# Kernel optimization log

Hardware: AMD Instinct MI355X
Metric: run time of the kernel (lower is better)

## Reference

```python
import jax, jax.numpy as jnp
import numpy as np

B, D, R, F = 4096, 14, 7, 768

def setup_inputs() -> dict:
    key = jax.random.key(0)
    ks = jax.random.split(key, 8)
    s = 1.0 / np.sqrt(F)
    return {
        "features": jax.random.normal(ks[0], (B, D, F), dtype=jnp.float32),
        "region_embeddings": jax.random.normal(ks[1], (R, F), dtype=jnp.float32),
        "Wq": jax.random.uniform(ks[2], (F, F), jnp.float32, -s, s),
        "bq": jnp.zeros((F,), jnp.float32),
        "Wk": jax.random.uniform(ks[3], (F, F), jnp.float32, -s, s),
        "bk": jnp.zeros((F,), jnp.float32),
        "Wv": jax.random.uniform(ks[4], (F, F), jnp.float32, -s, s),
        "bv": jnp.zeros((F,), jnp.float32),
        "region_weights": jnp.array([1.0, 1.0, 1.2, 1.5, 1.3, 1.1, 1.4], dtype=jnp.float32),
    }

def reference(features, region_embeddings, Wq, bq, Wk, bk, Wv, bv, region_weights):
    scale = features.shape[-1] ** -0.5
    # Q: [B, D, F]; K, V: [R, F] (shared across batch, broadcast instead of expand)
    Q = jnp.einsum('bdf,gf->bdg', features, Wq) + bq
    K = region_embeddings @ Wk.T + bk   # [R, F]
    V = region_embeddings @ Wv.T + bv   # [R, F]
    scores = jnp.einsum('bdf,rf->bdr', Q, K) * scale      # [B, D, R]
    scores = scores * region_weights[None, None, :]        # elementwise region bias
    attn = jax.nn.softmax(scores, axis=-1)                 # [B, D, R]
    attended = jnp.einsum('bdr,rf->bdf', attn, V)          # [B, D, F]
    return attended, attn
```

## Files before the change

kernel.cpp:

```cpp
#include <hip/hip_runtime.h>
#include <math.h>

#define FDIM 768
#define RNUM 7
#define BDIM 4096
#define DDIM 14
#define BD (BDIM * DDIM)
#define RF (RNUM * FDIM)
#define NCHUNK 4
#define GPC (FDIM / NCHUNK)
#define SCALE 0.03608439182435161f

#define CBLK 896
#define NW (CBLK * 8)
#define CITER 4

typedef float f4v __attribute__((ext_vector_type(4)));

#define DPP_ADD(x, ctrl)                                                      \
    x += __int_as_float(__builtin_amdgcn_update_dpp(                          \
        0, __float_as_int(x), ctrl, 0xf, 0xf, true))

__device__ __forceinline__ float wave_sum(float x)
{
    DPP_ADD(x, 0x111);
    DPP_ADD(x, 0x112);
    DPP_ADD(x, 0x114);
    DPP_ADD(x, 0x118);
    DPP_ADD(x, 0x142);
    DPP_ADD(x, 0x143);
    return __int_as_float(__builtin_amdgcn_readlane(__float_as_int(x), 63));
}

__global__ __launch_bounds__(512) void kv_kernel(
    const float* __restrict__ re,
    const float* __restrict__ Wk, const float* __restrict__ bk,
    const float* __restrict__ Wv, const float* __restrict__ bv,
    float* __restrict__ Kbuf, float* __restrict__ Vbuf,
    float* __restrict__ Kp, float* __restrict__ c_acc)
{
    __shared__ float re_s[RF];
    int tid = threadIdx.x;
    for (int i = tid; i < RF / 4; i += 512)
        ((float4*)re_s)[i] = ((const float4*)re)[i];

    if (blockIdx.x == 0) {
        float4 z = make_float4(0.f, 0.f, 0.f, 0.f);
        for (int i = tid; i < RF / 4; i += 512)
            ((float4*)Kp)[i] = z;
        if (tid < RNUM) c_acc[tid] = 0.f;
    }
    __syncthreads();

    int lane = tid & 63;
    int gwave = (int)((blockIdx.x * 512 + tid) >> 6);
    int which = gwave >= FDIM;
    int f = gwave - which * FDIM;

    const float4* W4 = (const float4*)((which ? Wv : Wk) + (size_t)f * FDIM);
    float4 w0 = W4[lane];
    float4 w1 = W4[lane + 64];
    float4 w2 = W4[lane + 128];

    float s[RNUM];
#pragma unroll
    for (int r = 0; r < RNUM; ++r) {
        const float4* a4 = (const float4*)(re_s + r * FDIM);
        float4 a0 = a4[lane];
        float4 a1 = a4[lane + 64];
        float4 a2 = a4[lane + 128];
        float p = a0.x * w0.x + a0.y * w0.y + a0.z * w0.z + a0.w * w0.w
                + a1.x * w1.x + a1.y * w1.y + a1.z * w1.z + a1.w * w1.w
                + a2.x * w2.x + a2.y * w2.y + a2.z * w2.z + a2.w * w2.w;
        s[r] = wave_sum(p);
    }

    float bias = which ? bv[f] : bk[f];
    float my = s[0];
#pragma unroll
    for (int r = 1; r < RNUM; ++r) my = (lane == r) ? s[r] : my;
    if (lane < RNUM)
        (which ? Vbuf : Kbuf)[(size_t)lane * FDIM + f] = my + bias;
}

__global__ __launch_bounds__(256) void kp_kernel(
    const float* __restrict__ Wq, const float* __restrict__ bq,
    const float* __restrict__ Kbuf,
    float* __restrict__ Kp, float* __restrict__ c_acc)
{
    const int bpc = 6;
    int chunk = blockIdx.x / bpc;
    int id = (blockIdx.x % bpc) * 256 + threadIdx.x;
    int g0 = chunk * GPC;

    if (id < RF / 4) {
        int r = id / (FDIM / 4);
        int f4i = id - r * (FDIM / 4);
        const float* kr = Kbuf + (size_t)r * FDIM + g0;
        f4v acc = {0.f, 0.f, 0.f, 0.f};
#pragma unroll 8
        for (int g = 0; g < GPC; ++g) {
            float kg = kr[g];
            f4v w = ((const f4v*)(Wq + (size_t)(g0 + g) * FDIM))[f4i];
            acc += kg * w;
        }
        float* dst = Kp + (size_t)id * 4;
        atomicAdd(dst + 0, acc.x);
        atomicAdd(dst + 1, acc.y);
        atomicAdd(dst + 2, acc.z);
        atomicAdd(dst + 3, acc.w);
    } else if (id < RF / 4 + RNUM) {
        int r = id - RF / 4;
        const float* kr = Kbuf + (size_t)r * FDIM + g0;
        const float* bqp = bq + g0;
        float sum = 0.f;
#pragma unroll 8
        for (int g = 0; g < GPC; ++g)
            sum += bqp[g] * kr[g];
        atomicAdd(c_acc + r, sum);
    }
}

__global__ __launch_bounds__(512, 2) void attn_kernel(
    const float* __restrict__ feat,
    const float* __restrict__ Kp, const float* __restrict__ c_acc,
    const float* __restrict__ Vbuf, const float* __restrict__ rw,
    float* __restrict__ out_att, float* __restrict__ out_attn)
{
    __shared__ float kp_s[RF];
    __shared__ float v_s[RF];
    __shared__ float c_s[RNUM];
    __shared__ float w_s[RNUM];

    int tid = threadIdx.x;
    int lane = tid & 63;
    int wave = (int)((blockIdx.x * 512 + tid) >> 6);
    int rb = wave;

    float4 x0[3], x1[3];
    {
        const float4* f0 = (const float4*)(feat + (size_t)rb * 2 * FDIM);
        const float4* f1 = (const float4*)(feat + ((size_t)rb * 2 + 1) * FDIM);
#pragma unroll
        for (int j = 0; j < 3; ++j) x0[j] = f0[lane + 64 * j];
#pragma unroll
        for (int j = 0; j < 3; ++j) x1[j] = f1[lane + 64 * j];
    }

    for (int i = tid; i < RF / 4; i += 512) {
        ((float4*)kp_s)[i] = ((const float4*)Kp)[i];
        ((float4*)v_s)[i] = ((const float4*)Vbuf)[i];
    }
    if (tid < RNUM) {
        c_s[tid] = c_acc[tid];
        w_s[tid] = rw[tid] * SCALE;
    }
    __syncthreads();

    float cw[RNUM], ww[RNUM];
#pragma unroll
    for (int r = 0; r < RNUM; ++r) {
        cw[r] = __int_as_float(__builtin_amdgcn_readfirstlane(__float_as_int(c_s[r])));
        ww[r] = __int_as_float(__builtin_amdgcn_readfirstlane(__float_as_int(w_s[r])));
    }

#pragma unroll 1
    for (int it = 0; it < CITER; ++it) {
        size_t row = (size_t)rb * 2;
        int rb_n = rb + NW;

        float p0[RNUM], p1[RNUM];
#pragma unroll
        for (int r = 0; r < RNUM; ++r) {
            const float4* kp4 = (const float4*)(kp_s + r * FDIM);
            float4 k0 = kp4[lane];
            float4 k1 = kp4[lane + 64];
            float4 k2 = kp4[lane + 128];
            p0[r] = x0[0].x * k0.x + x0[0].y * k0.y + x0[0].z * k0.z + x0[0].w * k0.w
                  + x0[1].x * k1.x + x0[1].y * k1.y + x0[1].z * k1.z + x0[1].w * k1.w
                  + x0[2].x * k2.x + x0[2].y * k2.y + x0[2].z * k2.z + x0[2].w * k2.w;
            p1[r] = x1[0].x * k0.x + x1[0].y * k0.y + x1[0].z * k0.z + x1[0].w * k0.w
                  + x1[1].x * k1.x + x1[1].y * k1.y + x1[1].z * k1.z + x1[1].w * k1.w
                  + x1[2].x * k2.x + x1[2].y * k2.y + x1[2].z * k2.z + x1[2].w * k2.w;
        }

        if (rb_n < BD / 2) {
            const float4* f0 = (const float4*)(feat + (size_t)rb_n * 2 * FDIM);
            const float4* f1 = (const float4*)(feat + ((size_t)rb_n * 2 + 1) * FDIM);
#pragma unroll
            for (int j = 0; j < 3; ++j) x0[j] = f0[lane + 64 * j];
#pragma unroll
            for (int j = 0; j < 3; ++j) x1[j] = f1[lane + 64 * j];
        }

        float s0[RNUM], s1[RNUM];
#pragma unroll
        for (int r = 0; r < RNUM; ++r) {
            s0[r] = (wave_sum(p0[r]) + cw[r]) * ww[r];
            s1[r] = (wave_sum(p1[r]) + cw[r]) * ww[r];
        }

        float mx0 = s0[0], mx1 = s1[0];
#pragma unroll
        for (int r = 1; r < RNUM; ++r) { mx0 = fmaxf(mx0, s0[r]); mx1 = fmaxf(mx1, s1[r]); }
        float d0 = 0.f, d1 = 0.f;
#pragma unroll
        for (int r = 0; r < RNUM; ++r) {
            s0[r] = __expf(s0[r] - mx0); d0 += s0[r];
            s1[r] = __expf(s1[r] - mx1); d1 += s1[r];
        }
        float i0 = 1.0f / d0, i1 = 1.0f / d1;
#pragma unroll
        for (int r = 0; r < RNUM; ++r) { s0[r] *= i0; s1[r] *= i1; }

        float4 o0[3], o1[3];
#pragma unroll
        for (int j = 0; j < 3; ++j) {
            o0[j] = make_float4(0.f, 0.f, 0.f, 0.f);
            o1[j] = make_float4(0.f, 0.f, 0.f, 0.f);
        }
#pragma unroll
        for (int r = 0; r < RNUM; ++r) {
            const float4* v4 = (const float4*)(v_s + r * FDIM);
            float4 va = v4[lane];
            float4 vb = v4[lane + 64];
            float4 vc = v4[lane + 128];
            float a0 = s0[r], a1 = s1[r];
            o0[0].x += a0 * va.x; o0[0].y += a0 * va.y; o0[0].z += a0 * va.z; o0[0].w += a0 * va.w;
            o0[1].x += a0 * vb.x; o0[1].y += a0 * vb.y; o0[1].z += a0 * vb.z; o0[1].w += a0 * vb.w;
            o0[2].x += a0 * vc.x; o0[2].y += a0 * vc.y; o0[2].z += a0 * vc.z; o0[2].w += a0 * vc.w;
            o1[0].x += a1 * va.x; o1[0].y += a1 * va.y; o1[0].z += a1 * va.z; o1[0].w += a1 * va.w;
            o1[1].x += a1 * vb.x; o1[1].y += a1 * vb.y; o1[1].z += a1 * vb.z; o1[1].w += a1 * vb.w;
            o1[2].x += a1 * vc.x; o1[2].y += a1 * vc.y; o1[2].z += a1 * vc.z; o1[2].w += a1 * vc.w;
        }
        f4v* q0 = (f4v*)(out_att + row * FDIM);
        f4v* q1 = (f4v*)(out_att + (row + 1) * FDIM);
#pragma unroll
        for (int j = 0; j < 3; ++j)
            __builtin_nontemporal_store(*(f4v*)&o0[j], q0 + lane + 64 * j);
#pragma unroll
        for (int j = 0; j < 3; ++j)
            __builtin_nontemporal_store(*(f4v*)&o1[j], q1 + lane + 64 * j);

        float my = s0[0];
#pragma unroll
        for (int r = 1; r < RNUM; ++r) my = (lane == r) ? s0[r] : my;
#pragma unroll
        for (int r = 0; r < RNUM; ++r) my = (lane == RNUM + r) ? s1[r] : my;
        if (lane < 2 * RNUM)
            __builtin_nontemporal_store(my, out_attn + row * RNUM + lane);

        rb = rb_n;
    }
}

extern "C" void kernel_launch(void* const* d_in, const int* in_sizes, int n_in,
                              void* d_out, int out_size, void* d_ws, size_t ws_size,
                              hipStream_t stream)
{
    const float* features = (const float*)d_in[0];
    const float* region_embeddings = (const float*)d_in[1];
    const float* Wq = (const float*)d_in[2];
    const float* bq = (const float*)d_in[3];
    const float* Wk = (const float*)d_in[4];
    const float* bk = (const float*)d_in[5];
    const float* Wv = (const float*)d_in[6];
    const float* bv = (const float*)d_in[7];
    const float* region_weights = (const float*)d_in[8];

    float* out = (float*)d_out;
    float* out_att  = out;
    float* out_attn = out + (size_t)BD * FDIM;

    float* Kbuf  = (float*)d_ws;
    float* Vbuf  = Kbuf + RF;
    float* Kp    = Vbuf + RF;
    float* c_acc = Kp + RF;

    {
        kv_kernel<<<192, 512, 0, stream>>>(region_embeddings, Wk, bk, Wv, bv,
                                           Kbuf, Vbuf, Kp, c_acc);
    }
    {
        kp_kernel<<<NCHUNK * 6, 256, 0, stream>>>(Wq, bq, Kbuf, Kp, c_acc);
    }
    {
        attn_kernel<<<CBLK, 512, 0, stream>>>(features, Kp, c_acc, Vbuf,
                                              region_weights, out_att, out_attn);
    }
}
```

Before: 77.90 us.

## Hold Kp in registers and process four rows per wave in attention kernel

Moves the projected key matrix from shared memory into per-lane registers and raises per-wave work from two rows to four per iteration, with smaller 256-thread blocks and more iterations. This is meant to remove repeated LDS reads of Kp and amortize the V reads and reductions over more rows. The cost is much higher register pressure, which may lower occupancy or cause spills in a memory-bound kernel.

After: 140.9 us. +80.9%, slower.

```diff
diff --git a/kernel.cpp b/kernel.cpp
--- a/kernel.cpp
+++ b/kernel.cpp
@@ -11,9 +11,9 @@
 #define GPC (FDIM / NCHUNK)
 #define SCALE 0.03608439182435161f
 
-#define CBLK 896
-#define NW (CBLK * 8)
-#define CITER 4
+#define CBLK 512
+#define CWAVES (CBLK * 4)
+#define CITER 7
 
 typedef float f4v __attribute__((ext_vector_type(4)));
 
@@ -121,36 +121,46 @@
     }
 }
 
-__global__ __launch_bounds__(512, 2) void attn_kernel(
+__global__ __launch_bounds__(256, 2) void attn_kernel(
     const float* __restrict__ feat,
     const float* __restrict__ Kp, const float* __restrict__ c_acc,
     const float* __restrict__ Vbuf, const float* __restrict__ rw,
     float* __restrict__ out_att, float* __restrict__ out_attn)
 {
-    __shared__ float kp_s[RF];
     __shared__ float v_s[RF];
     __shared__ float c_s[RNUM];
     __shared__ float w_s[RNUM];
 
     int tid = threadIdx.x;
     int lane = tid & 63;
-    int wave = (int)((blockIdx.x * 512 + tid) >> 6);
+    int wave = (int)((blockIdx.x * 256 + tid) >> 6);
     int rb = wave;
 
-    float4 x0[3], x1[3];
+    float4 x0[3], x1[3], x2[3], x3[3];
     {
-        const float4* f0 = (const float4*)(feat + (size_t)rb * 2 * FDIM);
-        const float4* f1 = (const float4*)(feat + ((size_t)rb * 2 + 1) * FDIM);
+        const float4* f0 = (const float4*)(feat + (size_t)rb * 4 * FDIM);
+        const float4* f1 = (const float4*)(feat + ((size_t)rb * 4 + 1) * FDIM);
+        const float4* f2 = (const float4*)(feat + ((size_t)rb * 4 + 2) * FDIM);
+        const float4* f3 = (const float4*)(feat + ((size_t)rb * 4 + 3) * FDIM);
 #pragma unroll
         for (int j = 0; j < 3; ++j) x0[j] = f0[lane + 64 * j];
 #pragma unroll
         for (int j = 0; j < 3; ++j) x1[j] = f1[lane + 64 * j];
-    }
-
-    for (int i = tid; i < RF / 4; i += 512) {
-        ((float4*)kp_s)[i] = ((const float4*)Kp)[i];
+#pragma unroll
+        for (int j = 0; j < 3; ++j) x2[j] = f2[lane + 64 * j];
+#pragma unroll
+        for (int j = 0; j < 3; ++j) x3[j] = f3[lane + 64 * j];
+    }
+
+    float4 kp[RNUM][3];
+#pragma unroll
+    for (int r = 0; r < RNUM; ++r)
+#pragma unroll
+        for (int j = 0; j < 3; ++j)
+            kp[r][j] = ((const float4*)Kp)[r * (FDIM / 4) + lane + 64 * j];
+
+    for (int i = tid; i < RF / 4; i += 256)
         ((float4*)v_s)[i] = ((const float4*)Vbuf)[i];
-    }
     if (tid < RNUM) {
         c_s[tid] = c_acc[tid];
         w_s[tid] = rw[tid] * SCALE;
@@ -166,88 +176,106 @@
 
 #pragma unroll 1
     for (int it = 0; it < CITER; ++it) {
-        size_t row = (size_t)rb * 2;
-        int rb_n = rb + NW;
-
-        float p0[RNUM], p1[RNUM];
+        size_t row = (size_t)rb * 4;
+        int rb_n = rb + CWAVES;
+
+        float p0[RNUM], p1[RNUM], p2[RNUM], p3[RNUM];
 #pragma unroll
         for (int r = 0; r < RNUM; ++r) {
-            const float4* kp4 = (const float4*)(kp_s + r * FDIM);
-            float4 k0 = kp4[lane];
-            float4 k1 = kp4[lane + 64];
-            float4 k2 = kp4[lane + 128];
+            float4 k0 = kp[r][0], k1 = kp[r][1], k2 = kp[r][2];
             p0[r] = x0[0].x * k0.x + x0[0].y * k0.y + x0[0].z * k0.z + x0[0].w * k0.w
                   + x0[1].x * k1.x + x0[1].y * k1.y + x0[1].z * k1.z + x0[1].w * k1.w
                   + x0[2].x * k2.x + x0[2].y * k2.y + x0[2].z * k2.z + x0[2].w * k2.w;
             p1[r] = x1[0].x * k0.x + x1[0].y * k0.y + x1[0].z * k0.z + x1[0].w * k0.w
                   + x1[1].x * k1.x + x1[1].y * k1.y + x1[1].z * k1.z + x1[1].w * k1.w
                   + x1[2].x * k2.x + x1[2].y * k2.y + x1[2].z * k2.z + x1[2].w * k2.w;
-        }
-
-        if (rb_n < BD / 2) {
-            const float4* f0 = (const float4*)(feat + (size_t)rb_n * 2 * FDIM);
-            const float4* f1 = (const float4*)(feat + ((size_t)rb_n * 2 + 1) * FDIM);
+            p2[r] = x2[0].x * k0.x + x2[0].y * k0.y + x2[0].z * k0.z + x2[0].w * k0.w
+                  + x2[1].x * k1.x + x2[1].y * k1.y + x2[1].z * k1.z + x2[1].w * k1.w
+                  + x2[2].x * k2.x + x2[2].y * k2.y + x2[2].z * k2.z + x2[2].w * k2.w;
+            p3[r] = x3[0].x * k0.x + x3[0].y * k0.y + x3[0].z * k0.z + x3[0].w * k0.w
+                  + x3[1].x * k1.x + x3[1].y * k1.y + x3[1].z * k1.z + x3[1].w * k1.w
+                  + x3[2].x * k2.x + x3[2].y * k2.y + x3[2].z * k2.z + x3[2].w * k2.w;
+        }
+
+        if (rb_n < BD / 4) {
+            const float4* f0 = (const float4*)(feat + (size_t)rb_n * 4 * FDIM);
+            const float4* f1 = (const float4*)(feat + ((size_t)rb_n * 4 + 1) * FDIM);
+            const float4* f2 = (const float4*)(feat + ((size_t)rb_n * 4 + 2) * FDIM);
+            const float4* f3 = (const float4*)(feat + ((size_t)rb_n * 4 + 3) * FDIM);
 #pragma unroll
             for (int j = 0; j < 3; ++j) x0[j] = f0[lane + 64 * j];
 #pragma unroll
             for (int j = 0; j < 3; ++j) x1[j] = f1[lane + 64 * j];
-        }
-
-        float s0[RNUM], s1[RNUM];
+#pragma unroll
+            for (int j = 0; j < 3; ++j) x2[j] = f2[lane + 64 * j];
+#pragma unroll
+            for (int j = 0; j < 3; ++j) x3[j] = f3[lane + 64 * j];
+        }
+
+        float s0[RNUM], s1[RNUM], s2[RNUM], s3[RNUM];
 #pragma unroll
         for (int r = 0; r < RNUM; ++r) {
             s0[r] = (wave_sum(p0[r]) + cw[r]) * ww[r];
             s1[r] = (wave_sum(p1[r]) + cw[r]) * ww[r];
-        }
-
-        float mx0 = s0[0], mx1 = s1[0];
-#pragma unroll
-        for (int r = 1; r < RNUM; ++r) { mx0 = fmaxf(mx0, s0[r]); mx1 = fmaxf(mx1, s1[r]); }
-        float d0 = 0.f, d1 = 0.f;
+            s2[r] = (wave_sum(p2[r]) + cw[r]) * ww[r];
+            s3[r] = (wave_sum(p3[r]) + cw[r]) * ww[r];
+        }
+
+        float mx0 = s0[0], mx1 = s1[0], mx2 = s2[0], mx3 = s3[0];
+#pragma unroll
+        for (int r = 1; r < RNUM; ++r) {
+            mx0 = fmaxf(mx0, s0[r]); mx1 = fmaxf(mx1, s1[r]);
+            mx2 = fmaxf(mx2, s2[r]); mx3 = fmaxf(mx3, s3[r]);
+        }
+        float d0 = 0.f, d1 = 0.f, d2 = 0.f, d3 = 0.f;
 #pragma unroll
         for (int r = 0; r < RNUM; ++r) {
             s0[r] = __expf(s0[r] - mx0); d0 += s0[r];
             s1[r] = __expf(s1[r] - mx1); d1 += s1[r];
-        }
-        float i0 = 1.0f / d0, i1 = 1.0f / d1;
-#pragma unroll
-        for (int r = 0; r < RNUM; ++r) { s0[r] *= i0; s1[r] *= i1; }
-
-        float4 o0[3], o1[3];
-#pragma unroll
-        for (int j = 0; j < 3; ++j) {
-            o0[j] = make_float4(0.f, 0.f, 0.f, 0.f);
-            o1[j] = make_float4(0.f, 0.f, 0.f, 0.f);
-        }
+            s2[r] = __expf(s2[r] - mx2); d2 += s2[r];
+            s3[r] = __expf(s3[r] - mx3); d3 += s3[r];
+        }
+        float i0 = 1.0f / d0, i1 = 1.0f / d1, i2 = 1.0f / d2, i3 = 1.0f / d3;
 #pragma unroll
         for (int r = 0; r < RNUM; ++r) {
-            const float4* v4 = (const float4*)(v_s + r * FDIM);
-            float4 va = v4[lane];
-            float4 vb = v4[lane + 64];
-            float4 vc = v4[lane + 128];
-            float a0 = s0[r], a1 = s1[r];
-            o0[0].x += a0 * va.x; o0[0].y += a0 * va.y; o0[0].z += a0 * va.z; o0[0].w += a0 * va.w;
-            o0[1].x += a0 * vb.x; o0[1].y += a0 * vb.y; o0[1].z += a0 * vb.z; o0[1].w += a0 * vb.w;
-            o0[2].x += a0 * vc.x; o0[2].y += a0 * vc.y; o0[2].z += a0 * vc.z; o0[2].w += a0 * vc.w;
-            o1[0].x += a1 * va.x; o1[0].y += a1 * va.y; o1[0].z += a1 * va.z; o1[0].w += a1 * va.w;
-            o1[1].x += a1 * vb.x; o1[1].y += a1 * vb.y; o1[1].z += a1 * vb.z; o1[1].w += a1 * vb.w;
-            o1[2].x += a1 * vc.x; o1[2].y += a1 * vc.y; o1[2].z += a1 * vc.z; o1[2].w += a1 * vc.w;
-        }
+            s0[r] *= i0; s1[r] *= i1; s2[r] *= i2; s3[r] *= i3;
+        }
+
         f4v* q0 = (f4v*)(out_att + row * FDIM);
         f4v* q1 = (f4v*)(out_att + (row + 1) * FDIM);
-#pragma unroll
-        for (int j = 0; j < 3; ++j)
-            __builtin_nontemporal_store(*(f4v*)&o0[j], q0 + lane + 64 * j);
-#pragma unroll
-        for (int j = 0; j < 3; ++j)
-            __builtin_nontemporal_store(*(f4v*)&o1[j], q1 + lane + 64 * j);
+        f4v* q2 = (f4v*)(out_att + (row + 2) * FDIM);
+        f4v* q3 = (f4v*)(out_att + (row + 3) * FDIM);
+#pragma unroll
+        for (int j = 0; j < 3; ++j) {
+            float4 a0 = make_float4(0.f, 0.f, 0.f, 0.f);
+            float4 a1 = make_float4(0.f, 0.f, 0.f, 0.f);
+            float4 a2 = make_float4(0.f, 0.f, 0.f, 0.f);
+            float4 a3 = make_float4(0.f, 0.f, 0.f, 0.f);
+#pragma unroll
+            for (int r = 0; r < RNUM; ++r) {
+                float4 v = ((const float4*)(v_s + r * FDIM))[lane + 64 * j];
+                float b0 = s0[r], b1 = s1[r], b2 = s2[r], b3 = s3[r];
+                a0.x += b0 * v.x; a0.y += b0 * v.y; a0.z += b0 * v.z; a0.w += b0 * v.w;
+                a1.x += b1 * v.x; a1.y += b1 * v.y; a1.z += b1 * v.z; a1.w += b1 * v.w;
+                a2.x += b2 * v.x; a2.y += b2 * v.y; a2.z += b2 * v.z; a2.w += b2 * v.w;
+                a3.x += b3 * v.x; a3.y += b3 * v.y; a3.z += b3 * v.z; a3.w += b3 * v.w;
+            }
+            __builtin_nontemporal_store(*(f4v*)&a0, q0 + lane + 64 * j);
+            __builtin_nontemporal_store(*(f4v*)&a1, q1 + lane + 64 * j);
+            __builtin_nontemporal_store(*(f4v*)&a2, q2 + lane + 64 * j);
+            __builtin_nontemporal_store(*(f4v*)&a3, q3 + lane + 64 * j);
+        }
 
         float my = s0[0];
 #pragma unroll
         for (int r = 1; r < RNUM; ++r) my = (lane == r) ? s0[r] : my;
 #pragma unroll
         for (int r = 0; r < RNUM; ++r) my = (lane == RNUM + r) ? s1[r] : my;
-        if (lane < 2 * RNUM)
+#pragma unroll
+        for (int r = 0; r < RNUM; ++r) my = (lane == 2 * RNUM + r) ? s2[r] : my;
+#pragma unroll
+        for (int r = 0; r < RNUM; ++r) my = (lane == 3 * RNUM + r) ? s3[r] : my;
+        if (lane < 4 * RNUM)
             __builtin_nontemporal_store(my, out_attn + row * RNUM + lane);
 
         rb = rb_n;
@@ -285,7 +313,7 @@
         kp_kernel<<<NCHUNK * 6, 256, 0, stream>>>(Wq, bq, Kbuf, Kp, c_acc);
     }
     {
-        attn_kernel<<<CBLK, 512, 0, stream>>>(features, Kp, c_acc, Vbuf,
+        attn_kernel<<<CBLK, 256, 0, stream>>>(features, Kp, c_acc, Vbuf,
                                               region_weights, out_att, out_attn);
     }
 }
```
